# Performance work log

Measured on AMD Instinct MI355X. Metric: run time of the kernel, lower is better.

The kernel has to match this reference:

```python
import jax, jax.numpy as jnp
import numpy as np

EPS = 1e-5
HID = 32
FUSED = 33 * 33 * 33  # 35937


def _subnet(x, gamma, beta, W1, b1, W2, b2, W3, b3):
    # BatchNorm1d in training mode: batch mean / biased variance
    mu = jnp.mean(x, axis=0)
    var = jnp.mean((x - mu) ** 2, axis=0)
    xn = (x - mu) / jnp.sqrt(var + EPS) * gamma + beta
    h = jax.nn.relu(xn @ W1 + b1)
    h = jax.nn.relu(h @ W2 + b2)
    return jax.nn.relu(h @ W3 + b3)


def _subnet_params(key, in_dim):
    ks = jax.random.split(key, 6)
    s_in = 1.0 / np.sqrt(in_dim)
    s_h = 1.0 / np.sqrt(HID)
    return dict(
        gamma=jnp.ones((in_dim,), jnp.float32),
        beta=jnp.zeros((in_dim,), jnp.float32),
        W1=jax.random.uniform(ks[0], (in_dim, HID), jnp.float32, -s_in, s_in),
        b1=jax.random.uniform(ks[1], (HID,), jnp.float32, -s_in, s_in),
        W2=jax.random.uniform(ks[2], (HID, HID), jnp.float32, -s_h, s_h),
        b2=jax.random.uniform(ks[3], (HID,), jnp.float32, -s_h, s_h),
        W3=jax.random.uniform(ks[4], (HID, HID), jnp.float32, -s_h, s_h),
        b3=jax.random.uniform(ks[5], (HID,), jnp.float32, -s_h, s_h),
    )


def setup_inputs() -> dict:
    key = jax.random.key(0)
    ks = jax.random.split(key, 10)
    B = 8192
    inp = {
        'US_x': jax.random.normal(ks[0], (B, 1024), jnp.float32),
        'CDFI_x': jax.random.normal(ks[1], (B, 1024), jnp.float32),
        'marker_x': jax.random.normal(ks[2], (B, 10), jnp.float32),
    }
    for pref, k, d in (('us', ks[3], 1024), ('cd', ks[4], 1024), ('mk', ks[5], 10)):
        for n, v in _subnet_params(k, d).items():
            inp[f'{pref}_{n}'] = v
    s1 = 1.0 / np.sqrt(FUSED)
    s2 = 1.0 / np.sqrt(33)
    inp['Wf1'] = jax.random.uniform(ks[6], (FUSED, 33), jnp.float32, -s1, s1)
    inp['bf1'] = jax.random.uniform(ks[7], (33,), jnp.float32, -s1, s1)
    inp['Wf2'] = jax.random.uniform(ks[8], (33, 5), jnp.float32, -s2, s2)
    inp['bf2'] = jax.random.uniform(ks[9], (5,), jnp.float32, -s2, s2)
    return inp


def reference(US_x, CDFI_x, marker_x,
              us_gamma, us_beta, us_W1, us_b1, us_W2, us_b2, us_W3, us_b3,
              cd_gamma, cd_beta, cd_W1, cd_b1, cd_W2, cd_b2, cd_W3, cd_b3,
              mk_gamma, mk_beta, mk_W1, mk_b1, mk_W2, mk_b2, mk_W3, mk_b3,
              Wf1, bf1, Wf2, bf2):
    B = US_x.shape[0]
    us_h = _subnet(US_x, us_gamma, us_beta, us_W1, us_b1, us_W2, us_b2, us_W3, us_b3)
    cd_h = _subnet(CDFI_x, cd_gamma, cd_beta, cd_W1, cd_b1, cd_W2, cd_b2, cd_W3, cd_b3)
    mk_h = _subnet(marker_x, mk_gamma, mk_beta, mk_W1, mk_b1, mk_W2, mk_b2, mk_W3, mk_b3)
    ones = jnp.ones((B, 1), jnp.float32)
    us1 = jnp.concatenate([ones, us_h], axis=1)   # [B,33]
    cd1 = jnp.concatenate([ones, cd_h], axis=1)   # [B,33]
    mk1 = jnp.concatenate([ones, mk_h], axis=1)   # [B,33]
    # fused[b,k,j,i] = mk1[b,k] * cd1[b,j] * us1[b,i]; flattened row-major
    fused = jnp.einsum('bk,bj,bi->bkji', mk1, cd1, us1).reshape(B, FUSED)
    h = jax.nn.relu(fused @ Wf1 + bf1)
    return jax.nn.sigmoid(h @ Wf2 + bf2)
```

## Files before the change

### kernel.cpp

```cpp
#include <hip/hip_runtime.h>
#include <hip/hip_bf16.h>
#include <math.h>

typedef __hip_bfloat16 bf16;
typedef __attribute__((ext_vector_type(4))) float f32x4;
typedef __attribute__((ext_vector_type(8))) short s16x8;

#define NB 8192
#define KP 1120
#define NP 1152

struct SubP {
    const float* x; const float* gamma; const float* beta;
    const float* W1; const float* b1; const float* W2; const float* b2;
    const float* W3; const float* b3;
    float* sum; float* sumsq; float* a; float* b1p; float* hout;
    int F;
};
struct SubP3 { SubP s[3]; };

__global__ void __launch_bounds__(256) stats3_kernel(SubP3 P) {
    const SubP p = P.s[blockIdx.z];
    int t = threadIdx.x;
    int row0 = blockIdx.x * 128;
    if (p.F == 1024) {
        f32x4 s = {0.f, 0.f, 0.f, 0.f}, s2 = {0.f, 0.f, 0.f, 0.f};
        const float* xp = p.x + (size_t)row0 * 1024 + t * 4;
        #pragma unroll 8
        for (int r = 0; r < 128; r++) {
            f32x4 v = *(const f32x4*)(xp + (size_t)r * 1024);
            s += v; s2 += v * v;
        }
        int f = t * 4;
        #pragma unroll
        for (int e = 0; e < 4; e++) {
            atomicAdd(&p.sum[f + e], s[e]);
            atomicAdd(&p.sumsq[f + e], s2[e]);
        }
    } else {
        __shared__ float ls[16], ls2[16];
        if (t < 16) { ls[t] = 0.f; ls2[t] = 0.f; }
        __syncthreads();
        int F = p.F;
        for (int idx = t; idx < 128 * F; idx += 256) {
            float v = p.x[(size_t)row0 * F + idx];
            int f = idx % 10;
            atomicAdd(&ls[f], v);
            atomicAdd(&ls2[f], v * v);
        }
        __syncthreads();
        if (t < F) { atomicAdd(&p.sum[t], ls[t]); atomicAdd(&p.sumsq[t], ls2[t]); }
    }
}

__global__ void prep3_kernel(SubP3 P) {
    const SubP p = P.s[blockIdx.y];
    int f0 = blockIdx.x * 32;
    if (f0 >= p.F) return;
    int t = threadIdx.x;
    __shared__ float c_sh[32];
    __shared__ float red[8][33];
    int fc = p.F - f0; if (fc > 32) fc = 32;
    if (t < 32) {
        float c = 0.f;
        if (t < fc) {
            int f = f0 + t;
            float mu  = p.sum[f]   * (1.f / 8192.f);
            float var = p.sumsq[f] * (1.f / 8192.f) - mu * mu;
            float a = p.gamma[f] * rsqrtf(var + 1e-5f);
            p.a[f] = a;
            c = p.beta[f] - mu * a;
        }
        c_sh[t] = c;
    }
    __syncthreads();
    int h = t & 31, g = t >> 5;
    float s = 0.f;
    for (int fi = g; fi < fc; fi += 8)
        s += c_sh[fi] * p.W1[(size_t)(f0 + fi) * 32 + h];
    red[g][h] = s;
    __syncthreads();
    if (t < 32) {
        float tot = 0.f;
        #pragma unroll
        for (int gg = 0; gg < 8; gg++) tot += red[gg][t];
        atomicAdd(&p.b1p[t], tot);
    }
}

__global__ void __launch_bounds__(256) subnet3_kernel(SubP3 P) {
    const SubP p = P.s[blockIdx.y];
    const int F = p.F;
    __shared__ float smem[5664];
    float* Xt  = smem;
    float* Wt  = smem + 2176;
    float* Red = smem;
    float* H1  = smem + 3456;
    float* W23 = smem + 4608;
    float* H2  = smem;

    int t = threadIdx.x;
    int row0 = blockIdx.x * 32;
    int kg = t >> 6;
    int lane = t & 63;
    int hg = lane & 7, h0 = hg * 4;
    int rg = (lane >> 3) & 3;
    int ks = lane >> 5;
    int kbase = (kg * 2 + ks) * 8;

    float acc[4][8] = {};

    for (int k0 = 0; k0 < F; k0 += 64) {
        int kc = F - k0; if (kc > 64) kc = 64;
        int kcp = (kc + 3) & ~3;
        __syncthreads();
        if (kc == 64) {
            #pragma unroll
            for (int i = 0; i < 2; i++) {
                int idx = t + i * 256;
                int r = idx >> 4, c4 = (idx & 15) * 4;
                *(f32x4*)&Xt[r * 68 + c4] = *(const f32x4*)&p.x[(size_t)(row0 + r) * F + k0 + c4];
            }
            #pragma unroll
            for (int i = 0; i < 2; i++) {
                int idx = t + i * 256;
                int kk = idx >> 3, h4 = (idx & 7) * 4;
                f32x4 w = *(const f32x4*)&p.W1[(size_t)(k0 + kk) * 32 + h4];
                float av = p.a[k0 + kk];
                w *= av;
                *(f32x4*)&Wt[kk * 36 + h4] = w;
            }
        } else {
            for (int idx = t; idx < 32 * kcp; idx += 256) {
                int r = idx / kcp, kk = idx - r * kcp;
                Xt[r * 68 + kk] = (kk < kc) ? p.x[(size_t)(row0 + r) * F + k0 + kk] : 0.f;
            }
            for (int idx = t; idx < kcp * 32; idx += 256) {
                int kk = idx >> 5, hh = idx & 31;
                Wt[kk * 36 + hh] = (kk < kc) ? p.a[k0 + kk] * p.W1[(size_t)(k0 + kk) * 32 + hh] : 0.f;
            }
        }
        __syncthreads();
        #pragma unroll
        for (int s = 0; s < 2; s++) {
            int kk = kbase + s * 4;
            if (kk < kcp) {
                f32x4 wv[4], xv[8];
                #pragma unroll
                for (int j = 0; j < 4; j++)  wv[j]  = *(const f32x4*)&Wt[(kk + j) * 36 + h0];
                #pragma unroll
                for (int ri = 0; ri < 8; ri++) xv[ri] = *(const f32x4*)&Xt[(rg + 4 * ri) * 68 + kk];
                #pragma unroll
                for (int j = 0; j < 4; j++)
                    #pragma unroll
                    for (int hi = 0; hi < 4; hi++) {
                        float w = wv[j][hi];
                        #pragma unroll
                        for (int ri = 0; ri < 8; ri++)
                            acc[hi][ri] = fmaf(w, xv[ri][j], acc[hi][ri]);
                    }
            }
        }
    }
    #pragma unroll
    for (int hi = 0; hi < 4; hi++)
        #pragma unroll
        for (int ri = 0; ri < 8; ri++)
            acc[hi][ri] += __shfl_xor(acc[hi][ri], 32);
    __syncthreads();
    if (kg > 0 && ks == 0) {
        #pragma unroll
        for (int ri = 0; ri < 8; ri++) {
            int r = rg + 4 * ri;
            f32x4 v = {acc[0][ri], acc[1][ri], acc[2][ri], acc[3][ri]};
            *(f32x4*)&Red[(kg - 1) * 1152 + r * 36 + h0] = v;
        }
    }
    for (int idx = t; idx < 1024; idx += 256) W23[(idx >> 5) * 33 + (idx & 31)] = p.W2[idx];
    __syncthreads();
    if (kg == 0 && ks == 0) {
        f32x4 b;
        #pragma unroll
        for (int hi = 0; hi < 4; hi++) b[hi] = p.b1[h0 + hi] + p.b1p[h0 + hi];
        #pragma unroll
        for (int ri = 0; ri < 8; ri++) {
            int r = rg + 4 * ri;
            f32x4 v = {acc[0][ri], acc[1][ri], acc[2][ri], acc[3][ri]};
            #pragma unroll
            for (int pp = 0; pp < 3; pp++)
                v += *(const f32x4*)&Red[pp * 1152 + r * 36 + h0];
            v += b;
            #pragma unroll
            for (int hi = 0; hi < 4; hi++)
                H1[r * 36 + h0 + hi] = fmaxf(v[hi], 0.f);
        }
    }
    __syncthreads();
    int h = t & 31, rq = t >> 5;
    {
        float a2[4] = {};
        for (int q = 0; q < 32; q++) {
            float w = W23[q * 33 + h];
            #pragma unroll
            for (int i = 0; i < 4; i++) a2[i] += H1[(rq * 4 + i) * 36 + q] * w;
        }
        float bv = p.b2[h];
        #pragma unroll
        for (int i = 0; i < 4; i++) H2[(rq * 4 + i) * 36 + h] = fmaxf(a2[i] + bv, 0.f);
    }
    __syncthreads();
    for (int idx = t; idx < 1024; idx += 256) W23[(idx >> 5) * 33 + (idx & 31)] = p.W3[idx];
    __syncthreads();
    {
        float a3[4] = {};
        for (int q = 0; q < 32; q++) {
            float w = W23[q * 33 + h];
            #pragma unroll
            for (int i = 0; i < 4; i++) a3[i] += H2[(rq * 4 + i) * 36 + q] * w;
        }
        float bv = p.b3[h];
        #pragma unroll
        for (int i = 0; i < 4; i++)
            p.hout[(size_t)(row0 + rq * 4 + i) * 32 + h] = fmaxf(a3[i] + bv, 0.f);
    }
}

__global__ void build_both(const float* __restrict__ mk_h, const float* __restrict__ us_h,
                           bf16* __restrict__ p1,
                           const float* __restrict__ Wf1, bf16* __restrict__ W2t) {
    int blk = blockIdx.x;
    int t = threadIdx.x;
    if (blk < NB) {
        int b = blk;
        __shared__ float mk1[33], us1[33];
        if (t == 0) { mk1[0] = 1.f; us1[0] = 1.f; }
        if (t < 32) mk1[t + 1] = mk_h[(size_t)b * 32 + t];
        else if (t < 64) us1[t - 31] = us_h[(size_t)b * 32 + (t - 32)];
        __syncthreads();
        if (t < 140) {
            int base = t * 8;
            s16x8 v;
            #pragma unroll
            for (int e = 0; e < 8; e++) {
                int idx = base + e;
                float val = 0.f;
                if (idx < 1089) {
                    int k = idx / 33, i = idx - k * 33;
                    val = mk1[k] * us1[i];
                }
                __hip_bfloat16 hb = __float2bfloat16(val);
                v[e] = *(short*)&hb;
            }
            *(s16x8*)(p1 + (size_t)b * KP + base) = v;
        }
    } else {
        int kj = blk - NB;
        int k = kj / 33, j = kj - k * 33;
        __shared__ float tile[1089];
        const float* src = Wf1 + (size_t)k * 35937 + (size_t)j * 1089;
        for (int idx = t; idx < 1089; idx += 192) tile[idx] = src[idx];
        __syncthreads();
        for (int idx = t; idx < 1089; idx += 192) {
            int o = idx / 33, i = idx - o * 33;
            W2t[(size_t)(j * 33 + o) * KP + k * 33 + i] = __float2bfloat16(tile[i * 33 + o]);
        }
    }
}

__global__ void __launch_bounds__(256) gemm_kernel(const bf16* __restrict__ A,
                                                   const bf16* __restrict__ Bt,
                                                   bf16* __restrict__ S) {
    __shared__ __align__(16) bf16 As[128 * 32];
    __shared__ __align__(16) bf16 Bs[128 * 32];
    int t = threadIdx.x;
    int m0 = blockIdx.x * 128;
    int n0 = blockIdx.y * 128;
    int wave = t >> 6, lane = t & 63;
    int wm = (wave & 1) * 64, wn = (wave >> 1) * 64;
    int fr = lane & 15;
    int kg = (lane >> 4) * 8;

    int lr = lane >> 2;
    int lk = (lane & 3) * 8;
    const bf16* Ag = A  + (size_t)(m0 + wave * 32 + lr) * KP + lk;
    const bf16* Bg = Bt + (size_t)(n0 + wave * 32 + lr) * KP + lk;
    bf16* AsW = As + wave * 32 * 32;
    bf16* BsW = Bs + wave * 32 * 32;

    f32x4 acc[4][4] = {};

    for (int k0 = 0; k0 < KP; k0 += 32) {
        __syncthreads();
        __builtin_amdgcn_global_load_lds(
            (const __attribute__((address_space(1))) void*)(Ag + k0),
            (__attribute__((address_space(3))) void*)(AsW), 16, 0, 0);
        __builtin_amdgcn_global_load_lds(
            (const __attribute__((address_space(1))) void*)(Ag + k0 + 16 * KP),
            (__attribute__((address_space(3))) void*)(AsW + 16 * 32), 16, 0, 0);
        __builtin_amdgcn_global_load_lds(
            (const __attribute__((address_space(1))) void*)(Bg + k0),
            (__attribute__((address_space(3))) void*)(BsW), 16, 0, 0);
        __builtin_amdgcn_global_load_lds(
            (const __attribute__((address_space(1))) void*)(Bg + k0 + 16 * KP),
            (__attribute__((address_space(3))) void*)(BsW + 16 * 32), 16, 0, 0);
        __syncthreads();
        s16x8 bfr[4];
        #pragma unroll
        for (int nt = 0; nt < 4; nt++)
            bfr[nt] = *(const s16x8*)(Bs + (wn + nt * 16 + fr) * 32 + kg);
        #pragma unroll
        for (int mt = 0; mt < 4; mt++) {
            s16x8 af = *(const s16x8*)(As + (wm + mt * 16 + fr) * 32 + kg);
            #pragma unroll
            for (int nt = 0; nt < 4; nt++)
                acc[mt][nt] = __builtin_amdgcn_mfma_f32_16x16x32_bf16(af, bfr[nt], acc[mt][nt], 0, 0, 0);
        }
    }
    int col = lane & 15, rowg = (lane >> 4) * 4;
    #pragma unroll
    for (int mt = 0; mt < 4; mt++)
        #pragma unroll
        for (int nt = 0; nt < 4; nt++)
            #pragma unroll
            for (int r = 0; r < 4; r++) {
                int gr = m0 + wm + mt * 16 + rowg + r;
                int gc = n0 + wn + nt * 16 + col;
                S[(size_t)gr * NP + gc] = __float2bfloat16(acc[mt][nt][r]);
            }
}

__global__ void __launch_bounds__(256) epilogue_kernel(const bf16* __restrict__ S,
                                const float* __restrict__ cd_h,
                                const float* __restrict__ bf1, const float* __restrict__ Wf2,
                                const float* __restrict__ bf2, float* __restrict__ out) {
    int w = threadIdx.x >> 6;
    int lane = threadIdx.x & 63;
    int b = blockIdx.x * 4 + w;
    __shared__ float Sl[4][1152];
    __shared__ float cdsh[4][33];
    __shared__ float hsh[4][40];
    const bf16* Srow = S + (size_t)b * NP;
    #pragma unroll
    for (int pass = 0; pass < 3; pass++) {
        int idx = lane + pass * 64;
        if (idx < 144) {
            s16x8 v = *(const s16x8*)(Srow + idx * 8);
            #pragma unroll
            for (int e = 0; e < 8; e++) {
                short sv = v[e];
                Sl[w][idx * 8 + e] = __bfloat162float(*(bf16*)&sv);
            }
        }
    }
    if (lane == 0) cdsh[w][0] = 1.f;
    if (lane < 32) cdsh[w][lane + 1] = cd_h[(size_t)b * 32 + lane];
    __syncthreads();
    if (lane < 33) {
        float acc = bf1[lane];
        #pragma unroll 3
        for (int j = 0; j < 33; j++)
            acc += cdsh[w][j] * Sl[w][j * 33 + lane];
        hsh[w][lane] = fmaxf(acc, 0.f);
    }
    __syncthreads();
    if (lane < 5) {
        float o = bf2[lane];
        for (int q = 0; q < 33; q++) o += hsh[w][q] * Wf2[q * 5 + lane];
        out[(size_t)b * 5 + lane] = 1.f / (1.f + expf(-o));
    }
}

extern "C" void kernel_launch(void* const* d_in, const int* in_sizes, int n_in,
                              void* d_out, int out_size, void* d_ws, size_t ws_size,
                              hipStream_t stream) {
    const float* US_x     = (const float*)d_in[0];
    const float* CDFI_x   = (const float*)d_in[1];
    const float* marker_x = (const float*)d_in[2];
    const float* Wf1      = (const float*)d_in[27];
    const float* bf1      = (const float*)d_in[28];
    const float* Wf2      = (const float*)d_in[29];
    const float* bf2      = (const float*)d_in[30];
    float* out = (float*)d_out;

    char* ws = (char*)d_ws;
    size_t off = 0;
    auto alloc = [&](size_t bytes) -> void* {
        void* p = ws + off;
        off = (off + bytes + 255) & ~(size_t)255;
        return p;
    };

    float* stat_big = (float*)alloc(3 * 2176 * sizeof(float));
    float* a_buf[3], *h_buf[3];
    for (int i = 0; i < 3; i++) {
        a_buf[i] = (float*)alloc(1024 * 4);
        h_buf[i] = (float*)alloc((size_t)NB * 32 * 4);
    }
    bf16*  p1   = (bf16*)alloc((size_t)NB * KP * 2);
    bf16*  W2t  = (bf16*)alloc((size_t)NP * KP * 2);
    bf16*  S    = (bf16*)alloc((size_t)NB * NP * 2);

    SubP3 P;
    const float* xs[3] = {US_x, CDFI_x, marker_x};
    int Fs[3] = {1024, 1024, 10};
    for (int i = 0; i < 3; i++) {
        int base = 3 + i * 8;
        P.s[i].x     = xs[i];
        P.s[i].gamma = (const float*)d_in[base + 0];
        P.s[i].beta  = (const float*)d_in[base + 1];
        P.s[i].W1    = (const float*)d_in[base + 2];
        P.s[i].b1    = (const float*)d_in[base + 3];
        P.s[i].W2    = (const float*)d_in[base + 4];
        P.s[i].b2    = (const float*)d_in[base + 5];
        P.s[i].W3    = (const float*)d_in[base + 6];
        P.s[i].b3    = (const float*)d_in[base + 7];
        P.s[i].sum   = stat_big + i * 2176;
        P.s[i].sumsq = stat_big + i * 2176 + 1024;
        P.s[i].b1p   = stat_big + i * 2176 + 2048;
        P.s[i].a     = a_buf[i];
        P.s[i].hout  = h_buf[i];
        P.s[i].F     = Fs[i];
    }

    float* us_h = h_buf[0];
    float* cd_h = h_buf[1];
    float* mk_h = h_buf[2];

    hipMemsetAsync(stat_big, 0, 3 * 2176 * sizeof(float), stream);
    hipMemsetAsync(W2t, 0, (size_t)NP * KP * 2, stream);

    stats3_kernel<<<dim3(64, 1, 3), 256, 0, stream>>>(P);
    prep3_kernel<<<dim3(32, 3), 256, 0, stream>>>(P);
    subnet3_kernel<<<dim3(256, 3), 256, 0, stream>>>(P);

    build_both<<<NB + 1089, 192, 0, stream>>>(mk_h, us_h, p1, Wf1, W2t);

    gemm_kernel<<<dim3(NB / 128, NP / 128), 256, 0, stream>>>(p1, W2t, S);

    epilogue_kernel<<<NB / 4, 256, 0, stream>>>(S, cd_h, bf1, Wf2, bf2, out);
}
```

Before: 270.8 us.

## Prefetch subnet tiles in registers, drop W2t memset, halve stats rows per block

For the 1024-feature subnets, the first-layer loop now uses 128-wide K chunks. The next chunk's x and W1 values are prefetched into registers while the current one is computed, which hides global load latency behind the math. The full W2t memset is replaced by explicit zeroing of the padding columns inside build_both, and the stats kernel launches twice as many blocks with half the rows each. The epilogue also keeps S in shared memory as bf16 instead of expanding it to float. These changes add register and shared-memory pressure (larger smem in subnet3) and rely on the padding-zeroing covering every column the GEMM reads.

```diff
diff --git a/kernel.cpp b/kernel.cpp
--- a/kernel.cpp
+++ b/kernel.cpp
@@ -22,12 +22,12 @@
 __global__ void __launch_bounds__(256) stats3_kernel(SubP3 P) {
     const SubP p = P.s[blockIdx.z];
     int t = threadIdx.x;
-    int row0 = blockIdx.x * 128;
+    int row0 = blockIdx.x * 64;
     if (p.F == 1024) {
         f32x4 s = {0.f, 0.f, 0.f, 0.f}, s2 = {0.f, 0.f, 0.f, 0.f};
         const float* xp = p.x + (size_t)row0 * 1024 + t * 4;
         #pragma unroll 8
-        for (int r = 0; r < 128; r++) {
+        for (int r = 0; r < 64; r++) {
             f32x4 v = *(const f32x4*)(xp + (size_t)r * 1024);
             s += v; s2 += v * v;
         }
@@ -42,7 +42,7 @@
         if (t < 16) { ls[t] = 0.f; ls2[t] = 0.f; }
         __syncthreads();
         int F = p.F;
-        for (int idx = t; idx < 128 * F; idx += 256) {
+        for (int idx = t; idx < 64 * F; idx += 256) {
             float v = p.x[(size_t)row0 * F + idx];
             int f = idx % 10;
             atomicAdd(&ls[f], v);
@@ -91,9 +91,7 @@
 __global__ void __launch_bounds__(256) subnet3_kernel(SubP3 P) {
     const SubP p = P.s[blockIdx.y];
     const int F = p.F;
-    __shared__ float smem[5664];
-    float* Xt  = smem;
-    float* Wt  = smem + 2176;
+    __shared__ float smem[8832];
     float* Red = smem;
     float* H1  = smem + 3456;
     float* W23 = smem + 4608;
@@ -106,50 +104,45 @@
     int hg = lane & 7, h0 = hg * 4;
     int rg = (lane >> 3) & 3;
     int ks = lane >> 5;
-    int kbase = (kg * 2 + ks) * 8;
 
     float acc[4][8] = {};
 
-    for (int k0 = 0; k0 < F; k0 += 64) {
-        int kc = F - k0; if (kc > 64) kc = 64;
-        int kcp = (kc + 3) & ~3;
-        __syncthreads();
-        if (kc == 64) {
-            #pragma unroll
-            for (int i = 0; i < 2; i++) {
-                int idx = t + i * 256;
-                int r = idx >> 4, c4 = (idx & 15) * 4;
-                *(f32x4*)&Xt[r * 68 + c4] = *(const f32x4*)&p.x[(size_t)(row0 + r) * F + k0 + c4];
-            }
-            #pragma unroll
-            for (int i = 0; i < 2; i++) {
-                int idx = t + i * 256;
-                int kk = idx >> 3, h4 = (idx & 7) * 4;
-                f32x4 w = *(const f32x4*)&p.W1[(size_t)(k0 + kk) * 32 + h4];
-                float av = p.a[k0 + kk];
-                w *= av;
-                *(f32x4*)&Wt[kk * 36 + h4] = w;
-            }
-        } else {
-            for (int idx = t; idx < 32 * kcp; idx += 256) {
-                int r = idx / kcp, kk = idx - r * kcp;
-                Xt[r * 68 + kk] = (kk < kc) ? p.x[(size_t)(row0 + r) * F + k0 + kk] : 0.f;
-            }
-            for (int idx = t; idx < kcp * 32; idx += 256) {
-                int kk = idx >> 5, hh = idx & 31;
-                Wt[kk * 36 + hh] = (kk < kc) ? p.a[k0 + kk] * p.W1[(size_t)(k0 + kk) * 32 + hh] : 0.f;
-            }
-        }
-        __syncthreads();
-        #pragma unroll
-        for (int s = 0; s < 2; s++) {
-            int kk = kbase + s * 4;
-            if (kk < kcp) {
+    if (F == 1024) {
+        float* Xt = smem;
+        float* Wt = smem + 4224;
+        int xr = t >> 3, xc = (t & 7) * 16;
+        int wk = t >> 1, wh = (t & 1) * 16;
+        const float* xbase = p.x + (size_t)row0 * 1024;
+        f32x4 xp[4], wp[4]; float av;
+        #pragma unroll
+        for (int i = 0; i < 4; i++) xp[i] = *(const f32x4*)&xbase[(size_t)xr * 1024 + xc + i * 4];
+        #pragma unroll
+        for (int i = 0; i < 4; i++) wp[i] = *(const f32x4*)&p.W1[(size_t)wk * 32 + wh + i * 4];
+        av = p.a[wk];
+        int kb = (kg * 2 + ks) * 16;
+        for (int c = 0; c < 8; c++) {
+            __syncthreads();
+            #pragma unroll
+            for (int i = 0; i < 4; i++) *(f32x4*)&Xt[xr * 132 + xc + i * 4] = xp[i];
+            #pragma unroll
+            for (int i = 0; i < 4; i++) *(f32x4*)&Wt[wk * 36 + wh + i * 4] = wp[i] * av;
+            if (c < 7) {
+                int k0 = (c + 1) * 128;
+                #pragma unroll
+                for (int i = 0; i < 4; i++) xp[i] = *(const f32x4*)&xbase[(size_t)xr * 1024 + k0 + xc + i * 4];
+                #pragma unroll
+                for (int i = 0; i < 4; i++) wp[i] = *(const f32x4*)&p.W1[(size_t)(k0 + wk) * 32 + wh + i * 4];
+                av = p.a[k0 + wk];
+            }
+            __syncthreads();
+            #pragma unroll
+            for (int s = 0; s < 4; s++) {
+                int kk = kb + s * 4;
                 f32x4 wv[4], xv[8];
                 #pragma unroll
                 for (int j = 0; j < 4; j++)  wv[j]  = *(const f32x4*)&Wt[(kk + j) * 36 + h0];
                 #pragma unroll
-                for (int ri = 0; ri < 8; ri++) xv[ri] = *(const f32x4*)&Xt[(rg + 4 * ri) * 68 + kk];
+                for (int ri = 0; ri < 8; ri++) xv[ri] = *(const f32x4*)&Xt[(rg + 4 * ri) * 132 + kk];
                 #pragma unroll
                 for (int j = 0; j < 4; j++)
                     #pragma unroll
@@ -159,6 +152,44 @@
                         for (int ri = 0; ri < 8; ri++)
                             acc[hi][ri] = fmaf(w, xv[ri][j], acc[hi][ri]);
                     }
+            }
+        }
+    } else {
+        float* Xt = smem;
+        float* Wt = smem + 2176;
+        int kbase = (kg * 2 + ks) * 8;
+        for (int k0 = 0; k0 < F; k0 += 64) {
+            int kc = F - k0; if (kc > 64) kc = 64;
+            int kcp = (kc + 3) & ~3;
+            __syncthreads();
+            for (int idx = t; idx < 32 * kcp; idx += 256) {
+                int r = idx / kcp, kk = idx - r * kcp;
+                Xt[r * 68 + kk] = (kk < kc) ? p.x[(size_t)(row0 + r) * F + k0 + kk] : 0.f;
+            }
+            for (int idx = t; idx < kcp * 32; idx += 256) {
+                int kk = idx >> 5, hh = idx & 31;
+                Wt[kk * 36 + hh] = (kk < kc) ? p.a[k0 + kk] * p.W1[(size_t)(k0 + kk) * 32 + hh] : 0.f;
+            }
+            __syncthreads();
+            #pragma unroll
+            for (int s = 0; s < 2; s++) {
+                int kk = kbase + s * 4;
+                if (kk < kcp) {
+                    f32x4 wv[4], xv[8];
+                    #pragma unroll
+                    for (int j = 0; j < 4; j++)  wv[j]  = *(const f32x4*)&Wt[(kk + j) * 36 + h0];
+                    #pragma unroll
+                    for (int ri = 0; ri < 8; ri++) xv[ri] = *(const f32x4*)&Xt[(rg + 4 * ri) * 68 + kk];
+                    #pragma unroll
+                    for (int j = 0; j < 4; j++)
+                        #pragma unroll
+                        for (int hi = 0; hi < 4; hi++) {
+                            float w = wv[j][hi];
+                            #pragma unroll
+                            for (int ri = 0; ri < 8; ri++)
+                                acc[hi][ri] = fmaf(w, xv[ri][j], acc[hi][ri]);
+                        }
+                }
             }
         }
     }
@@ -263,6 +294,13 @@
         for (int idx = t; idx < 1089; idx += 192) {
             int o = idx / 33, i = idx - o * 33;
             W2t[(size_t)(j * 33 + o) * KP + k * 33 + i] = __float2bfloat16(tile[i * 33 + o]);
+        }
+        if (k == 0) {
+            bf16 z = __float2bfloat16(0.f);
+            for (int idx = t; idx < 33 * 31; idx += 192) {
+                int o = idx / 31, kkp = 1089 + idx - o * 31;
+                W2t[(size_t)(j * 33 + o) * KP + kkp] = z;
+            }
         }
     }
 }
@@ -336,21 +374,15 @@
     int w = threadIdx.x >> 6;
     int lane = threadIdx.x & 63;
     int b = blockIdx.x * 4 + w;
-    __shared__ float Sl[4][1152];
+    __shared__ __align__(16) unsigned short Sl[4][1152];
     __shared__ float cdsh[4][33];
     __shared__ float hsh[4][40];
     const bf16* Srow = S + (size_t)b * NP;
     #pragma unroll
     for (int pass = 0; pass < 3; pass++) {
         int idx = lane + pass * 64;
-        if (idx < 144) {
-            s16x8 v = *(const s16x8*)(Srow + idx * 8);
-            #pragma unroll
-            for (int e = 0; e < 8; e++) {
-                short sv = v[e];
-                Sl[w][idx * 8 + e] = __bfloat162float(*(bf16*)&sv);
-            }
-        }
+        if (idx < 144)
+            *(s16x8*)&Sl[w][idx * 8] = *(const s16x8*)(Srow + idx * 8);
     }
     if (lane == 0) cdsh[w][0] = 1.f;
     if (lane < 32) cdsh[w][lane + 1] = cd_h[(size_t)b * 32 + lane];
@@ -358,8 +390,10 @@
     if (lane < 33) {
         float acc = bf1[lane];
         #pragma unroll 3
-        for (int j = 0; j < 33; j++)
-            acc += cdsh[w][j] * Sl[w][j * 33 + lane];
+        for (int j = 0; j < 33; j++) {
+            unsigned short sv = Sl[w][j * 33 + lane];
+            acc += cdsh[w][j] * __bfloat162float(*(bf16*)&sv);
+        }
         hsh[w][lane] = fmaxf(acc, 0.f);
     }
     __syncthreads();
@@ -427,9 +461,8 @@
     float* mk_h = h_buf[2];
 
     hipMemsetAsync(stat_big, 0, 3 * 2176 * sizeof(float), stream);
-    hipMemsetAsync(W2t, 0, (size_t)NP * KP * 2, stream);
-
-    stats3_kernel<<<dim3(64, 1, 3), 256, 0, stream>>>(P);
+
+    stats3_kernel<<<dim3(128, 1, 3), 256, 0, stream>>>(P);
     prep3_kernel<<<dim3(32, 3), 256, 0, stream>>>(P);
     subnet3_kernel<<<dim3(256, 3), 256, 0, stream>>>(P);
 
```

Result: faster. 261.8 us (-3.3%).
